# Kernel optimization log

Measured on AMD Instinct MI355X. Metric: run time of the kernel, lower is better.

Reference implementation:

```python
import jax, jax.numpy as jnp
import numpy as np

PD = 3                      # spatial feature dim (z, y, x)
HB = 1024                   # hash base per lattice coordinate
HOFF = 512                  # offset: lattice coords assumed in [-512, 511]
FILL = np.int32(2**31 - 1)  # sentinel for padded hash slots
EPS = 2.220446049250313e-16 # np.finfo('float').eps as in the torch module

def _elev_mat():
    # Embedding onto hyperplane sum(x)=0 with std-dev scale factors
    # (canonical permutohedral-lattice elevation, Adams et al.).
    E = np.zeros((PD + 1, PD), np.float32)
    E[0] = 1.0
    for i in range(1, PD + 1):
        E[i, i - 1] = -i
        E[i, i:] = 1.0
    inv_std = np.sqrt(2.0 / 3.0) * (PD + 1)
    scale = inv_std / np.sqrt(np.arange(1, PD + 1) * np.arange(2, PD + 2))
    return (E * scale[None, :]).astype(np.float32)

_EMAT = _elev_mat()
_IU = np.triu(np.ones((PD + 1, PD + 1), bool), 1)   # j > i
_IL = np.tril(np.ones((PD + 1, PD + 1), bool), -1)  # j < i

def _hash(k):  # (..., PD) int32 -> (...,) int32, injective for |coord| < 512
    return ((k[..., 0] + HOFF) * HB + (k[..., 1] + HOFF)) * HB + (k[..., 2] + HOFF)

def permutohedral(values, features):
    """Splat-blur-slice Gaussian filter. values (N,VD), features (N,PD)."""
    N, VD = values.shape
    elevated = features @ jnp.asarray(_EMAT).T                  # (N, PD+1)
    # nearest remainder-0 lattice point (nearest multiple of PD+1, ties -> down)
    v = elevated / (PD + 1)
    up, down = jnp.ceil(v), jnp.floor(v)
    rem0 = jnp.where(up - v < v - down, up, down) * (PD + 1)
    diff = elevated - rem0
    lt = diff[:, :, None] < diff[:, None, :]
    le = diff[:, :, None] <= diff[:, None, :]
    rank = (lt & _IU).sum(-1) + (le & _IL).sum(-1)              # (N, PD+1) int32
    rank = rank + jnp.round(rem0.sum(-1) / (PD + 1)).astype(rank.dtype)[:, None]
    shift = jnp.where(rank < 0, PD + 1, 0) + jnp.where(rank > PD, -(PD + 1), 0)
    rank = rank + shift
    rem0 = rem0 + shift.astype(rem0.dtype)
    # barycentric coordinates inside the enclosing simplex
    t = (elevated - rem0) / (PD + 1)                            # (N, PD+1)
    ohA = jax.nn.one_hot(PD - rank, PD + 2, dtype=values.dtype)
    ohB = jax.nn.one_hot(PD + 1 - rank, PD + 2, dtype=values.dtype)
    b = (ohA * t[..., None]).sum(1) - (ohB * t[..., None]).sum(1)
    b = b.at[:, 0].add(1.0 + b[:, PD + 1])
    bary = b[:, :PD + 1]                                        # (N, PD+1)
    # keys of the PD+1 simplex vertices (first PD coords; last is implied)
    rem0i = rem0[:, :PD].astype(jnp.int32)
    ranki = rank[:, :PD].astype(jnp.int32)
    r = jnp.arange(PD + 1, dtype=jnp.int32)[None, :, None]
    keys = rem0i[:, None, :] + jnp.where(ranki[:, None, :] >= PD + 1 - r, r - (PD + 1), r)  # (N,PD+1,PD)
    h = _hash(keys).reshape(-1)                                 # (N*(PD+1),)
    M = h.shape[0]
    uh, inv = jnp.unique(h, size=M, fill_value=FILL, return_inverse=True)
    inv = inv.reshape(-1)
    # splat
    contrib = (values[:, None, :] * bary[:, :, None]).reshape(M, VD)
    lat = jax.ops.segment_sum(contrib, inv, num_segments=M)     # (M, VD)
    # decode unique keys from the (invertible) hash
    k2 = uh % HB - HOFF
    tq = uh // HB
    k1 = tq % HB - HOFF
    k0 = tq // HB - HOFF
    ukeys = jnp.stack([k0, k1, k2], -1).astype(jnp.int32)       # (M, PD)
    valid = (uh != FILL)[:, None]
    # blur with [0.5, 1, 0.5] along each of the PD+1 lattice directions
    def lookup(nk, lat_):
        nh = _hash(nk)
        idx = jnp.clip(jnp.searchsorted(uh, nh), 0, M - 1)
        ok = (uh[idx] == nh)[:, None]
        return jnp.where(ok, lat_[idx], 0.0)
    for j in range(PD + 1):
        o = np.ones(PD, np.int32)
        if j < PD:
            o[j] = -PD
        o = jnp.asarray(o)
        lat = jnp.where(valid, lat + 0.5 * (lookup(ukeys + o, lat) + lookup(ukeys - o, lat)), 0.0)
    # slice
    alpha = 1.0 / (1.0 + 2.0 ** (-PD))
    return alpha * jnp.einsum('nr,nrv->nv', bary, lat[inv.reshape(-1, PD + 1)])

def spatial_features(image, v_gamma, sigma_gamma):
    _, d, h, w = image.shape
    z = jnp.arange(d, dtype=jnp.float32)[:, None, None]
    y = jnp.arange(h, dtype=jnp.float32)[None, :, None]
    x = jnp.arange(w, dtype=jnp.float32)[None, None, :]
    zz = v_gamma[0] * jnp.broadcast_to(z, (d, h, w)) / sigma_gamma[0]
    xx = v_gamma[1] * jnp.broadcast_to(x, (d, h, w)) / sigma_gamma[1]
    yy = v_gamma[2] * jnp.broadcast_to(y, (d, h, w)) / sigma_gamma[2]
    return jnp.stack([zz, yy, xx], axis=3)                      # (d,h,w,3)

def setup_inputs() -> dict:
    key = jax.random.key(0)
    k1, k2 = jax.random.split(key)
    C, D, H, W = 4, 64, 128, 128
    return {
        'input_': jax.random.normal(k1, (C, D, H, W), jnp.float32),
        'image': jax.random.normal(k2, (1, D, H, W), jnp.float32),
        'v_gamma': jnp.ones((3,), jnp.float32),       # nn.Parameter init [1,1,1]
        'sigma_gamma': 5.0 * jnp.ones((3,), jnp.float32),
    }

def reference(input_, image, v_gamma, sigma_gamma):
    C, d, h, w = input_.shape
    N = d * h * w
    feats = spatial_features(image, v_gamma, sigma_gamma).reshape(N, PD)
    # filter q and the all-ones normalizer in one pass (linear per channel)
    vals = jnp.concatenate([input_.reshape(C, N).T, jnp.ones((N, 1), jnp.float32)], axis=1)
    out = permutohedral(vals, feats)
    q = out[:, :C].T.reshape(C, d, h, w)
    norm = out[:, C].reshape(1, d, h, w)
    return q * (1.0 / (norm + EPS))
```

## Files before the change

### kernel.cpp

```cpp
#include <hip/hip_runtime.h>


#define DD    64
#define HHH   128
#define WWW   128
#define NPTS  (DD * HHH * WWW)
#define LATN  (1 << 17)
#define LATF  (LATN * 5)
#define DQ    7
#define CELLS (DQ * DQ * DQ * 4)
#define MASKW ((CELLS + 31) / 32)

__device__ __forceinline__ int encK(int K0, int K1, int K2) {
    return ((K2 >> 2) << 12) | ((K1 >> 2) << 7) | ((K0 >> 2) << 2) | (K0 & 3);
}

__device__ __forceinline__ void pl_geom(int z, int y, int x,
                                        const float* __restrict__ vg,
                                        const float* __restrict__ sg,
                                        int* Kout , float* bout) {
    float f0 = vg[0] * (float)z / sg[0];
    float f1 = vg[2] * (float)y / sg[2];
    float f2 = vg[1] * (float)x / sg[1];

    const float m00 = (float)2.3094010767585034;
    const float m01 = (float)1.3333333333333333;
    const float m02 = (float)0.9428090415820634;
    const float m21 = (float)-2.6666666666666665;
    const float m32 = (float)-2.8284271247461903;

    float e[4];
    e[0] =  m00 * f0 + m01 * f1 + m02 * f2;
    e[1] = -m00 * f0 + m01 * f1 + m02 * f2;
    e[2] =  m21 * f1 + m02 * f2;
    e[3] =  m32 * f2;

    float rem0[4];
    int sumr = 0;
    #pragma unroll
    for (int i = 0; i < 4; ++i) {
        float v = e[i] * 0.25f;
        float up = ceilf(v), dn = floorf(v);
        float rr = ((up - v) < (v - dn)) ? up : dn;
        rem0[i] = rr * 4.0f;
        sumr += (int)rem0[i];
    }
    sumr /= 4;

    float diff[4];
    #pragma unroll
    for (int i = 0; i < 4; ++i) diff[i] = e[i] - rem0[i];
    int rank[4] = {0, 0, 0, 0};
    #pragma unroll
    for (int i = 0; i < 4; ++i)
        #pragma unroll
        for (int j = i + 1; j < 4; ++j) {
            if (diff[i] < diff[j]) rank[i]++; else rank[j]++;
        }

    #pragma unroll
    for (int i = 0; i < 4; ++i) {
        rank[i] += sumr;
        if (rank[i] < 0)      { rank[i] += 4; rem0[i] += 4.0f; }
        else if (rank[i] > 3) { rank[i] -= 4; rem0[i] -= 4.0f; }
    }

    float b[5] = {0.f, 0.f, 0.f, 0.f, 0.f};
    #pragma unroll
    for (int i = 0; i < 4; ++i) {
        float t = (e[i] - rem0[i]) * 0.25f;
        b[3 - rank[i]] += t;
        b[4 - rank[i]] -= t;
    }
    b[0] += 1.0f + b[4];

    int k0 = (int)rem0[0] + 16, k1 = (int)rem0[1] + 48, k2 = (int)rem0[2] + 88;
    #pragma unroll
    for (int r = 0; r < 4; ++r) {
        int o0 = (rank[0] >= 4 - r) ? (r - 4) : r;
        int o1 = (rank[1] >= 4 - r) ? (r - 4) : r;
        int o2 = (rank[2] >= 4 - r) ? (r - 4) : r;
        Kout[r * 3 + 0] = k0 + o0;
        Kout[r * 3 + 1] = k1 + o1;
        Kout[r * 3 + 2] = k2 + o2;
        bout[r] = b[r];
    }
}

__device__ __forceinline__ void pl_claim(int key, unsigned int* __restrict__ exists,
                                         int* __restrict__ wcnt, int* __restrict__ wl) {
    if (atomicExch(&exists[key], 1u) == 0u) {
        int p = atomicAdd(wcnt, 1);
        wl[p] = key;
    }
}

__device__ __forceinline__ int make_id(const int* K, int B0, int B1, int B2) {
    int l0 = K[0] - B0, l1 = K[1] - B1, l2 = K[2] - B2;
    if (((unsigned)l0 < 4u * DQ) & ((unsigned)l1 < 4u * DQ) & ((unsigned)l2 < 4u * DQ))
        return ((((l2 >> 2) * DQ) + (l1 >> 2)) * DQ + (l0 >> 2)) * 4 + (l0 & 3);
    return ~encK(K[0] & 127, K[1] & 127, K[2] & 127);
}

__device__ __forceinline__ void pl_emit(int id, const float* a,
                                        float* sacc, unsigned int* smask,
                                        float* __restrict__ mycopy,
                                        unsigned int* __restrict__ exists,
                                        int* __restrict__ wcnt, int* __restrict__ wl) {
    if (id >= 0) {
        #pragma unroll
        for (int c = 0; c < 5; ++c) atomicAdd(&sacc[id * 5 + c], a[c]);
        atomicOr(&smask[id >> 5], 1u << (id & 31));
    } else {
        int key = ~id;
        float* L = mycopy + (size_t)key * 5;
        #pragma unroll
        for (int c = 0; c < 5; ++c) atomicAdd(L + c, a[c]);
        pl_claim(key, exists, wcnt, wl);
    }
}

__global__ __launch_bounds__(256, 4)
void pl_splat(const float* __restrict__ vals, const float* __restrict__ vg,
              const float* __restrict__ sg, float* __restrict__ latc,
              unsigned int* __restrict__ exists,
              int* __restrict__ wcnt, int* __restrict__ wl) {
    __shared__ float sacc[CELLS * 5];
    __shared__ unsigned int smask[MASKW];
    for (int i = threadIdx.x; i < CELLS * 5; i += 256) sacc[i] = 0.f;
    for (int i = threadIdx.x; i < MASKW; i += 256) smask[i] = 0u;
    __syncthreads();

    int bt = blockIdx.x;
    int tx = (bt & 3) << 5;
    int ty = ((bt >> 2) & 15) << 3;
    int tz = (bt >> 6) << 2;

    float s0 = vg[0] / sg[0], s1 = vg[2] / sg[2], s2 = vg[1] / sg[1];
    const float m00 = 2.30940104f, m01 = 1.33333325f, m02 = 0.942809045f,
                m21 = -2.66666651f;
    float A0z = m00 * s0, A0y = m01 * s1, A0x = m02 * s2;
    float A1z = -A0z,     A1y = A0y,      A1x = A0x;
    float A2y = m21 * s1, A2x = A0x;
    float e0o = A0z * tz + A0y * ty + A0x * tx;
    float e1o = A1z * tz + A1y * ty + A1x * tx;
    float e2o = A2y * ty + A2x * tx;
    float e0m = e0o + fminf(0.f, A0z) * 3 + fminf(0.f, A0y) * 7 + fminf(0.f, A0x) * 31;
    float e1m = e1o + fminf(0.f, A1z) * 3 + fminf(0.f, A1y) * 7 + fminf(0.f, A1x) * 31;
    float e2m = e2o + fminf(0.f, A2y) * 7 + fminf(0.f, A2x) * 31;
    int B0 = ((int)floorf(e0m + 16.f - 7.f)) & ~3;
    int B1 = ((int)floorf(e1m + 48.f - 7.f)) & ~3;
    int B2 = ((int)floorf(e2m + 88.f - 7.f)) & ~3;

    int xs = threadIdx.x & 7;
    int xsl = ((xs & 3) << 1) | (xs >> 2);
    int x0 = tx + (xsl << 2);
    int y  = ty + ((threadIdx.x >> 3) & 7);
    int z  = tz + (threadIdx.x >> 6);
    int n0 = (z << 14) + (y << 7) + x0;

    float4 q0 = *(const float4*)(vals + n0);
    float4 q1 = *(const float4*)(vals + NPTS + n0);
    float4 q2 = *(const float4*)(vals + 2 * NPTS + n0);
    float4 q3 = *(const float4*)(vals + 3 * NPTS + n0);
    float ch0[4] = {q0.x, q0.y, q0.z, q0.w};
    float ch1[4] = {q1.x, q1.y, q1.z, q1.w};
    float ch2[4] = {q2.x, q2.y, q2.z, q2.w};
    float ch3[4] = {q3.x, q3.y, q3.z, q3.w};

    float* mycopy = latc + (size_t)(blockIdx.x & 3) * LATF;

    int cid[4];
    float acc[4][5];
    {
        int K[12]; float b[4];
        pl_geom(z, y, x0, vg, sg, K, b);
        #pragma unroll
        for (int r = 0; r < 4; ++r) {
            cid[r] = make_id(K + r * 3, B0, B1, B2);
            float w = b[r];
            acc[r][0] = w * ch0[0]; acc[r][1] = w * ch1[0];
            acc[r][2] = w * ch2[0]; acc[r][3] = w * ch3[0];
            acc[r][4] = w;
        }
    }
    #pragma unroll
    for (int p = 1; p < 4; ++p) {
        int K[12]; float b[4];
        pl_geom(z, y, x0 + p, vg, sg, K, b);
        #pragma unroll
        for (int r = 0; r < 4; ++r) {
            int id = make_id(K + r * 3, B0, B1, B2);
            float w = b[r];
            if (id == cid[r]) {
                acc[r][0] += w * ch0[p]; acc[r][1] += w * ch1[p];
                acc[r][2] += w * ch2[p]; acc[r][3] += w * ch3[p];
                acc[r][4] += w;
            } else {
                pl_emit(cid[r], acc[r], sacc, smask, mycopy, exists, wcnt, wl);
                cid[r] = id;
                acc[r][0] = w * ch0[p]; acc[r][1] = w * ch1[p];
                acc[r][2] = w * ch2[p]; acc[r][3] = w * ch3[p];
                acc[r][4] = w;
            }
        }
    }
    #pragma unroll
    for (int r = 0; r < 4; ++r)
        pl_emit(cid[r], acc[r], sacc, smask, mycopy, exists, wcnt, wl);

    __syncthreads();

    for (int i = threadIdx.x; i < CELLS; i += 256) {
        if (!((smask[i >> 5] >> (i & 31)) & 1u)) continue;
        int r = i & 3, q = i >> 2;
        int l0q = q % DQ; int t = q / DQ;
        int l1q = t % DQ; int l2q = t / DQ;
        int K0 = B0 + (l0q << 2) + r;
        int K1 = B1 + (l1q << 2) + r;
        int K2 = B2 + (l2q << 2) + r;
        int key = encK(K0 & 127, K1 & 127, K2 & 127);
        pl_claim(key, exists, wcnt, wl);
        float* L = mycopy + (size_t)key * 5;
        #pragma unroll
        for (int c = 0; c < 5; ++c) atomicAdd(L + c, sacc[i * 5 + c]);
    }
}

__global__ __launch_bounds__(256)
void pl_blur(const unsigned int* __restrict__ exists,
             const int* __restrict__ wl, const int* __restrict__ wcnt,
             const float* __restrict__ in, float* __restrict__ out,
             int d0, int d1, int d2, int first) {
    int total = (*wcnt) * 5;
    for (int i = blockIdx.x * 256 + threadIdx.x; i < total; i += 256 * 256) {
        int ci = i / 5, c = i - ci * 5;
        int didx = wl[ci];
        int r  = didx & 3;
        int K0 = (((didx >> 2)  & 31) << 2) | r;
        int K1 = (((didx >> 7)  & 31) << 2) | r;
        int K2 = (((didx >> 12) & 31) << 2) | r;
        size_t o = (size_t)didx * 5 + c;
        float ctr, n = 0.f;
        if (first)
            ctr = in[o] + in[LATF + o] + in[2 * LATF + o] + in[3 * LATF + o];
        else
            ctr = in[o];
        #pragma unroll
        for (int sgn = 0; sgn < 2; ++sgn) {
            int P0 = K0 + (sgn ? -d0 : d0);
            int P1 = K1 + (sgn ? -d1 : d1);
            int P2 = K2 + (sgn ? -d2 : d2);
            if (((unsigned)P0 < 128u) & ((unsigned)P1 < 128u) & ((unsigned)P2 < 128u)) {
                int nk = encK(P0, P1, P2);
                if (exists[nk]) {
                    size_t no = (size_t)nk * 5 + c;
                    if (first)
                        n += in[no] + in[LATF + no] + in[2 * LATF + no] + in[3 * LATF + no];
                    else
                        n += in[no];
                }
            }
        }
        out[o] = ctr + 0.5f * n;
    }
}

__global__ __launch_bounds__(256)
void pl_slice(const float* __restrict__ vg, const float* __restrict__ sg,
              const float* __restrict__ lat, float* __restrict__ out) {
    int n = blockIdx.x * 256 + threadIdx.x;
    if (n >= NPTS) return;
    int z = n >> 14;
    int y = (n >> 7) & 127;
    int x = n & 127;
    int K[12]; float b[4];
    pl_geom(z, y, x, vg, sg, K, b);
    float a0 = 0.f, a1 = 0.f, a2 = 0.f, a3 = 0.f, a4 = 0.f;
    #pragma unroll
    for (int r = 0; r < 4; ++r) {
        float w = b[r];
        int key = encK(K[r * 3] & 127, K[r * 3 + 1] & 127, K[r * 3 + 2] & 127);
        const float* L = lat + (size_t)key * 5;
        a0 += w * L[0]; a1 += w * L[1]; a2 += w * L[2]; a3 += w * L[3]; a4 += w * L[4];
    }
    const float alpha = (float)(1.0 / 1.125);
    float norm = alpha * a4 + (float)2.220446049250313e-16;
    float invn = 1.0f / norm;
    out[n]            = (alpha * a0) * invn;
    out[NPTS + n]     = (alpha * a1) * invn;
    out[2 * NPTS + n] = (alpha * a2) * invn;
    out[3 * NPTS + n] = (alpha * a3) * invn;
}

extern "C" void kernel_launch(void* const* d_in, const int* in_sizes, int n_in,
                              void* d_out, int out_size, void* d_ws, size_t ws_size,
                              hipStream_t stream) {
    const float* input = (const float*)d_in[0];
    const float* vg = (const float*)d_in[2];
    const float* sg = (const float*)d_in[3];
    float* out = (float*)d_out;

    char* ws = (char*)d_ws;
    float* latc = (float*)ws;
    unsigned int* exists = (unsigned int*)(latc + (size_t)4 * LATF);
    int* wcnt = (int*)(exists + LATN);
    int*   wl = (int*)(wcnt + 64);
    float* A  = (float*)(wl + LATN);
    float* B  = A + LATF;

    size_t zbytes = (size_t)4 * LATF * 4 + (size_t)LATN * 4 + 256;
    hipMemsetAsync(ws, 0, zbytes, stream);

    pl_splat<<<1024, dim3(256), 0, stream>>>(input, vg, sg, latc, exists, wcnt, wl);

    pl_blur<<<256, dim3(256), 0, stream>>>(exists, wl, wcnt, latc, A, -3, 1, 1, 1);
    pl_blur<<<256, dim3(256), 0, stream>>>(exists, wl, wcnt, A, B, 1, -3, 1, 0);
    pl_blur<<<256, dim3(256), 0, stream>>>(exists, wl, wcnt, B, A, 1, 1, -3, 0);
    pl_blur<<<256, dim3(256), 0, stream>>>(exists, wl, wcnt, A, B, 1, 1, 1, 0);

    pl_slice<<<NPTS / 256, dim3(256), 0, stream>>>(vg, sg, B, out);
}
```

Measured before the change: 154.7 us.

## Fuse four blur passes with grid barrier and enlarge splat tiles

Merges the four separate blur kernel launches into one persistent kernel of 64 blocks that uses a software grid barrier (atomic counter with spin-wait) between passes, which removes inter-kernel launch gaps. The splat kernel now uses 512-thread blocks covering twice the z depth, so each block accumulates more points into shared memory before flushing to global atomics. The trade-off is that only 64 blocks run the blur, which limits parallelism and memory-level throughput. The grid barrier also depends on all 64 blocks being resident at the same time.

After: 206.7 us. +33.6%, slower.

```diff
diff --git a/kernel.cpp b/kernel.cpp
--- a/kernel.cpp
+++ b/kernel.cpp
@@ -10,6 +10,7 @@
 #define DQ    7
 #define CELLS (DQ * DQ * DQ * 4)
 #define MASKW ((CELLS + 31) / 32)
+#define BLURG 64
 
 __device__ __forceinline__ int encK(int K0, int K1, int K2) {
     return ((K2 >> 2) << 12) | ((K1 >> 2) << 7) | ((K0 >> 2) << 2) | (K0 & 3);
@@ -120,21 +121,23 @@
     }
 }
 
-__global__ __launch_bounds__(256, 4)
+__global__ __launch_bounds__(512, 4)
 void pl_splat(const float* __restrict__ vals, const float* __restrict__ vg,
               const float* __restrict__ sg, float* __restrict__ latc,
               unsigned int* __restrict__ exists,
               int* __restrict__ wcnt, int* __restrict__ wl) {
-    __shared__ float sacc[CELLS * 5];
+    __shared__ float4 sacc4[CELLS * 5 / 4];
     __shared__ unsigned int smask[MASKW];
-    for (int i = threadIdx.x; i < CELLS * 5; i += 256) sacc[i] = 0.f;
-    for (int i = threadIdx.x; i < MASKW; i += 256) smask[i] = 0u;
+    float* sacc = (float*)sacc4;
+    for (int i = threadIdx.x; i < CELLS * 5 / 4; i += 512)
+        sacc4[i] = make_float4(0.f, 0.f, 0.f, 0.f);
+    if (threadIdx.x < MASKW) smask[threadIdx.x] = 0u;
     __syncthreads();
 
     int bt = blockIdx.x;
     int tx = (bt & 3) << 5;
     int ty = ((bt >> 2) & 15) << 3;
-    int tz = (bt >> 6) << 2;
+    int tz = (bt >> 6) << 3;
 
     float s0 = vg[0] / sg[0], s1 = vg[2] / sg[2], s2 = vg[1] / sg[1];
     const float m00 = 2.30940104f, m01 = 1.33333325f, m02 = 0.942809045f,
@@ -145,8 +148,8 @@
     float e0o = A0z * tz + A0y * ty + A0x * tx;
     float e1o = A1z * tz + A1y * ty + A1x * tx;
     float e2o = A2y * ty + A2x * tx;
-    float e0m = e0o + fminf(0.f, A0z) * 3 + fminf(0.f, A0y) * 7 + fminf(0.f, A0x) * 31;
-    float e1m = e1o + fminf(0.f, A1z) * 3 + fminf(0.f, A1y) * 7 + fminf(0.f, A1x) * 31;
+    float e0m = e0o + fminf(0.f, A0z) * 7 + fminf(0.f, A0y) * 7 + fminf(0.f, A0x) * 31;
+    float e1m = e1o + fminf(0.f, A1z) * 7 + fminf(0.f, A1y) * 7 + fminf(0.f, A1x) * 31;
     float e2m = e2o + fminf(0.f, A2y) * 7 + fminf(0.f, A2x) * 31;
     int B0 = ((int)floorf(e0m + 16.f - 7.f)) & ~3;
     int B1 = ((int)floorf(e1m + 48.f - 7.f)) & ~3;
@@ -211,7 +214,7 @@
 
     __syncthreads();
 
-    for (int i = threadIdx.x; i < CELLS; i += 256) {
+    for (int i = threadIdx.x; i < CELLS; i += 512) {
         if (!((smask[i >> 5] >> (i & 31)) & 1u)) continue;
         int r = i & 3, q = i >> 2;
         int l0q = q % DQ; int t = q / DQ;
@@ -227,13 +230,24 @@
     }
 }
 
-__global__ __launch_bounds__(256)
-void pl_blur(const unsigned int* __restrict__ exists,
-             const int* __restrict__ wl, const int* __restrict__ wcnt,
-             const float* __restrict__ in, float* __restrict__ out,
-             int d0, int d1, int d2, int first) {
-    int total = (*wcnt) * 5;
-    for (int i = blockIdx.x * 256 + threadIdx.x; i < total; i += 256 * 256) {
+__device__ __forceinline__ void gbar(int* cnt, int nblk) {
+    __syncthreads();
+    __threadfence();
+    if (threadIdx.x == 0) {
+        __hip_atomic_fetch_add(cnt, 1, __ATOMIC_RELEASE, __HIP_MEMORY_SCOPE_AGENT);
+        while (__hip_atomic_load(cnt, __ATOMIC_ACQUIRE, __HIP_MEMORY_SCOPE_AGENT) < nblk)
+            __builtin_amdgcn_s_sleep(2);
+    }
+    __syncthreads();
+    __threadfence();
+}
+
+__device__ __forceinline__ void blur_pass(const unsigned int* __restrict__ exists,
+                                          const int* __restrict__ wl, int cnt5,
+                                          const float* __restrict__ in,
+                                          float* __restrict__ out,
+                                          int d0, int d1, int d2, int first) {
+    for (int i = blockIdx.x * 256 + threadIdx.x; i < cnt5; i += BLURG * 256) {
         int ci = i / 5, c = i - ci * 5;
         int didx = wl[ci];
         int r  = didx & 3;
@@ -267,6 +281,21 @@
 }
 
 __global__ __launch_bounds__(256)
+void pl_blur_fused(const unsigned int* __restrict__ exists,
+                   const int* __restrict__ wl, const int* __restrict__ wcnt,
+                   const float* __restrict__ latc, float* __restrict__ A,
+                   float* __restrict__ B, int* __restrict__ bar) {
+    int cnt5 = (*wcnt) * 5;
+    blur_pass(exists, wl, cnt5, latc, A, -3, 1, 1, 1);
+    gbar(bar + 0, BLURG);
+    blur_pass(exists, wl, cnt5, A, B, 1, -3, 1, 0);
+    gbar(bar + 1, BLURG);
+    blur_pass(exists, wl, cnt5, B, A, 1, 1, -3, 0);
+    gbar(bar + 2, BLURG);
+    blur_pass(exists, wl, cnt5, A, B, 1, 1, 1, 0);
+}
+
+__global__ __launch_bounds__(256)
 void pl_slice(const float* __restrict__ vg, const float* __restrict__ sg,
               const float* __restrict__ lat, float* __restrict__ out) {
     int n = blockIdx.x * 256 + threadIdx.x;
@@ -305,6 +334,7 @@
     float* latc = (float*)ws;
     unsigned int* exists = (unsigned int*)(latc + (size_t)4 * LATF);
     int* wcnt = (int*)(exists + LATN);
+    int* bar  = wcnt + 4;
     int*   wl = (int*)(wcnt + 64);
     float* A  = (float*)(wl + LATN);
     float* B  = A + LATF;
@@ -312,12 +342,7 @@
     size_t zbytes = (size_t)4 * LATF * 4 + (size_t)LATN * 4 + 256;
     hipMemsetAsync(ws, 0, zbytes, stream);
 
-    pl_splat<<<1024, dim3(256), 0, stream>>>(input, vg, sg, latc, exists, wcnt, wl);
-
-    pl_blur<<<256, dim3(256), 0, stream>>>(exists, wl, wcnt, latc, A, -3, 1, 1, 1);
-    pl_blur<<<256, dim3(256), 0, stream>>>(exists, wl, wcnt, A, B, 1, -3, 1, 0);
-    pl_blur<<<256, dim3(256), 0, stream>>>(exists, wl, wcnt, B, A, 1, 1, -3, 0);
-    pl_blur<<<256, dim3(256), 0, stream>>>(exists, wl, wcnt, A, B, 1, 1, 1, 0);
-
+    pl_splat<<<512, dim3(512), 0, stream>>>(input, vg, sg, latc, exists, wcnt, wl);
+    pl_blur_fused<<<BLURG, dim3(256), 0, stream>>>(exists, wl, wcnt, latc, A, B, bar);
     pl_slice<<<NPTS / 256, dim3(256), 0, stream>>>(vg, sg, B, out);
 }
```
